# Kernel tuning notes

Measured on AMD Instinct MI355X. Metric: run time of the kernel, lower is better.

The kernel has to match this reference:

```python
import jax, jax.numpy as jnp
import numpy as np

NUM_HEADS = 16
LN_EPS = 1e-05


def setup_inputs() -> dict:
    key = jax.random.key(0)
    ks = jax.random.split(key, 10)
    B, S, H = 2, 2048, 1024
    s = 1.0 / np.sqrt(H)
    return {
        "hidden_states": jax.random.normal(ks[0], (B, S, H), dtype=jnp.float32),
        "Wq": jax.random.normal(ks[1], (H, H), dtype=jnp.float32) * s,
        "bq": jax.random.normal(ks[2], (H,), dtype=jnp.float32) * 0.02,
        "Wk": jax.random.normal(ks[3], (H, H), dtype=jnp.float32) * s,
        "bk": jax.random.normal(ks[4], (H,), dtype=jnp.float32) * 0.02,
        "Wv": jax.random.normal(ks[5], (H, H), dtype=jnp.float32) * s,
        "bv": jax.random.normal(ks[6], (H,), dtype=jnp.float32) * 0.02,
        "Wd": jax.random.normal(ks[7], (H, H), dtype=jnp.float32) * s,
        "bd": jax.random.normal(ks[8], (H,), dtype=jnp.float32) * 0.02,
        "ln_gamma": jnp.ones((H,), dtype=jnp.float32),
        "ln_beta": jnp.zeros((H,), dtype=jnp.float32),
    }


def reference(hidden_states, Wq, bq, Wk, bk, Wv, bv, Wd, bd, ln_gamma, ln_beta):
    B, S, H = hidden_states.shape
    nh = NUM_HEADS
    hd = H // nh

    # QKV projections (torch Linear: x @ W.T + b), split heads -> [B, nh, S, hd]
    def proj(W, b):
        y = jnp.einsum('bsh,oh->bso', hidden_states, W) + b
        return y.reshape(B, S, nh, hd).transpose(0, 2, 1, 3)

    q = proj(Wq, bq)
    k = proj(Wk, bk)
    v = proj(Wv, bv)

    # scaled dot-product attention: [B, nh, S, S]
    scores = jnp.einsum('bhqd,bhkd->bhqk', q, k) / jnp.sqrt(jnp.float32(hd))
    probs = jax.nn.softmax(scores, axis=-1)
    ctx = jnp.einsum('bhqk,bhkd->bhqd', probs, v)  # [B, nh, S, hd]
    ctx = ctx.transpose(0, 2, 1, 3).reshape(B, S, H)

    # output dense + residual + LayerNorm
    attn_out = jnp.einsum('bsh,oh->bso', ctx, Wd) + bd
    x = attn_out + hidden_states
    mu = jnp.mean(x, axis=-1, keepdims=True)
    var = jnp.mean(jnp.square(x - mu), axis=-1, keepdims=True)
    return (x - mu) * jax.lax.rsqrt(var + LN_EPS) * ln_gamma + ln_beta
```

## Files before the change

### kernel.cpp

```cpp
#include <hip/hip_runtime.h>

constexpr int kH    = 1024;
constexpr int kSEQ  = 2048;
constexpr int kBATCH= 2;
constexpr int kNH   = 16;
constexpr int kHD   = 64;
constexpr int kM    = 4096;

typedef _Float16 h8  __attribute__((ext_vector_type(8)));
typedef _Float16 h4  __attribute__((ext_vector_type(4)));
typedef float   f32x4 __attribute__((ext_vector_type(4)));

static __device__ __forceinline__ f32x4 mfma16(h8 a, h8 b, f32x4 c) {
  return __builtin_amdgcn_mfma_f32_16x16x32_f16(a, b, c, 0, 0, 0);
}

static __device__ __forceinline__ void gll16(const _Float16* g, _Float16* l) {
  __builtin_amdgcn_global_load_lds(
      (const __attribute__((address_space(1))) void*)g,
      (__attribute__((address_space(3))) void*)l, 16, 0, 0);
}

#define QSCALE 0.18033688011112042f
#define C0INIT (-5.770780163555854f)

__global__ __launch_bounds__(256) void cvt_all(
    const float* __restrict__ X,  const float* __restrict__ Wq,
    const float* __restrict__ Wk, const float* __restrict__ Wv,
    const float* __restrict__ Wd,
    _Float16* __restrict__ Xh,  _Float16* __restrict__ Wqh,
    _Float16* __restrict__ Wkh, _Float16* __restrict__ Wvh,
    _Float16* __restrict__ Wdh)
{
  int i = blockIdx.x * 256 + threadIdx.x;
  const float* src; _Float16* dst; int off;
  if (i < (kM * kH) / 4) {
    src = X; dst = Xh; off = i;
  } else {
    int j = i - (kM * kH) / 4;
    int w = j >> 18;
    off = j & 262143;
    src = (w == 0) ? Wq : (w == 1) ? Wk : (w == 2) ? Wv : Wd;
    dst = (w == 0) ? Wqh : (w == 1) ? Wkh : (w == 2) ? Wvh : Wdh;
  }
  float4 v = reinterpret_cast<const float4*>(src)[off];
  h4 o;
  o[0] = (_Float16)v.x; o[1] = (_Float16)v.y;
  o[2] = (_Float16)v.z; o[3] = (_Float16)v.w;
  reinterpret_cast<h4*>(dst)[off] = o;
}

__global__ __launch_bounds__(256, 3) void qkv_gemm(
    const _Float16* __restrict__ Xh,
    const _Float16* __restrict__ Wq, const _Float16* __restrict__ Wk,
    const _Float16* __restrict__ Wv,
    const float* __restrict__ bq, const float* __restrict__ bk,
    const float* __restrict__ bv,
    _Float16* __restrict__ Qo, _Float16* __restrict__ Ko, _Float16* __restrict__ Vo)
{
  const int bid = blockIdx.x;
  const int swz = (bid & 7) * 96 + (bid >> 3);
  const int bx  = swz & 7;
  const int rem = swz >> 3;
  const int by  = rem & 31;
  const int proj= rem >> 5;

  const _Float16* W   = (proj == 0) ? Wq : ((proj == 1) ? Wk : Wv);
  const float*    bias= (proj == 0) ? bq : ((proj == 1) ? bk : bv);
  _Float16*       Out = (proj == 0) ? Qo : ((proj == 1) ? Ko : Vo);

  const int m0 = by * 128, n0 = bx * 128;
  __shared__ __align__(16) char qsmem[32768];
  _Float16* const As = (_Float16*)qsmem;
  _Float16* const Bs = (_Float16*)(qsmem + 16384);
  _Float16* const Lt = (_Float16*)qsmem;

  const int tid  = threadIdx.x;
  const int wave = tid >> 6, lane = tid & 63, quad = lane >> 4, l16 = lane & 15;
  const int mw = (wave & 1) * 64, nw = (wave >> 1) * 64;

  f32x4 acc[4][4] = {};
  const int grow = wave * 32 + (lane >> 2);
  const int gcol = (lane & 3) * 8;
  const _Float16* Ag = Xh + (size_t)(m0 + grow) * kH + gcol;
  const _Float16* Bg = W  + (size_t)(n0 + grow) * kH + gcol;

  {
    gll16(Ag,            &As[wave * 1024]);
    gll16(Ag + 16 * kH,  &As[wave * 1024 + 512]);
    gll16(Bg,            &Bs[wave * 1024]);
    gll16(Bg + 16 * kH,  &Bs[wave * 1024 + 512]);
  }

  for (int k = 0; k < 32; ++k) {
    const int cur = k & 1;
    __syncthreads();
    if (k < 31) {
      const int k0 = (k + 1) * 32, nb = cur ^ 1;
      gll16(Ag + k0,           &As[nb * 4096 + wave * 1024]);
      gll16(Ag + 16 * kH + k0, &As[nb * 4096 + wave * 1024 + 512]);
      gll16(Bg + k0,           &Bs[nb * 4096 + wave * 1024]);
      gll16(Bg + 16 * kH + k0, &Bs[nb * 4096 + wave * 1024 + 512]);
    }
    h8 af[4], bf[4];
    #pragma unroll
    for (int mi = 0; mi < 4; ++mi)
      af[mi] = *reinterpret_cast<const h8*>(&As[cur * 4096 + (mw + mi * 16 + l16) * 32 + quad * 8]);
    #pragma unroll
    for (int ni = 0; ni < 4; ++ni)
      bf[ni] = *reinterpret_cast<const h8*>(&Bs[cur * 4096 + (nw + ni * 16 + l16) * 32 + quad * 8]);
    #pragma unroll
    for (int mi = 0; mi < 4; ++mi)
      #pragma unroll
      for (int ni = 0; ni < 4; ++ni)
        acc[mi][ni] = mfma16(af[mi], bf[ni], acc[mi][ni]);
  }

  if (proj != 2) {
    #pragma unroll
    for (int mi = 0; mi < 4; ++mi)
    #pragma unroll
    for (int ni = 0; ni < 4; ++ni) {
      const int ng = n0 + nw + ni * 16 + l16;
      const float bv_ = bias[ng];
      const int hh = ng >> 6, dd = ng & 63;
      #pragma unroll
      for (int r = 0; r < 4; ++r) {
        const int mg = m0 + mw + mi * 16 + quad * 4 + r;
        float val = acc[mi][ni][r] + bv_;
        if (proj == 0) val *= QSCALE;
        const int bb = mg >> 11, srow = mg & 2047;
        Out[(((size_t)(bb * kNH + hh) * kSEQ) + srow) * kHD + dd] = (_Float16)val;
      }
    }
  } else {
    __syncthreads();
    #pragma unroll
    for (int mi = 0; mi < 4; ++mi)
    #pragma unroll
    for (int ni = 0; ni < 4; ++ni) {
      const int ng = n0 + nw + ni * 16 + l16;
      const float bv_ = bias[ng];
      const int nl = nw + ni * 16 + l16;
      const int c16 = (mw >> 3) + mi * 2 + (quad >> 1);
      const int cs = c16 ^ (nl & 15);
      h4 pp;
      pp[0] = (_Float16)(acc[mi][ni][0] + bv_);
      pp[1] = (_Float16)(acc[mi][ni][1] + bv_);
      pp[2] = (_Float16)(acc[mi][ni][2] + bv_);
      pp[3] = (_Float16)(acc[mi][ni][3] + bv_);
      *reinterpret_cast<h4*>(&Lt[nl * 128 + cs * 8 + (quad & 1) * 4]) = pp;
    }
    __syncthreads();
    const int bb = m0 >> 11, srow0 = m0 & 2047;
    const int nl2 = tid >> 1, half = tid & 1;
    const int ng2 = n0 + nl2, hh2 = ng2 >> 6, dd2 = ng2 & 63;
    _Float16* dst = Out + ((size_t)(bb * kNH + hh2) * kHD + dd2) * kSEQ
                        + srow0 + half * 64;
    const int hperm = dd2 & 15;
    const int hx = hperm >> 1;
    const bool hswap = (hperm & 1);
    #pragma unroll
    for (int j = 0; j < 8; ++j) {
      const int c = half * 8 + j;
      const int cs = c ^ (nl2 & 15);
      h8 v = *reinterpret_cast<const h8*>(&Lt[nl2 * 128 + cs * 8]);
      if (hswap) {
        h8 vs;
        vs[0] = v[4]; vs[1] = v[5]; vs[2] = v[6]; vs[3] = v[7];
        vs[4] = v[0]; vs[5] = v[1]; vs[6] = v[2]; vs[7] = v[3];
        v = vs;
      }
      *reinterpret_cast<h8*>(dst + (j ^ hx) * 8) = v;
    }
  }
}

__global__ __launch_bounds__(512, 4) void attn_kernel(
    const _Float16* __restrict__ Q, const _Float16* __restrict__ K,
    const _Float16* __restrict__ Vt, _Float16* __restrict__ Ctx)
{
  const int bid = blockIdx.x;
  const int swzb = (bid & 7) * 64 + (bid >> 3);
  const int qt = swzb & 15, bh = swzb >> 4;
  const int tid = threadIdx.x;
  const int wave = tid >> 6, lane = tid & 63, quad = lane >> 4, l16 = lane & 15;
  const int sw = l16 & 7;
  const int qw = wave & 3;
  const int wg = wave >> 2;

  __shared__ __align__(16) char smem[49152];
  _Float16* const Kl = (_Float16*)smem;
  _Float16* const Vl = (_Float16*)(smem + 24576);
  float* const Ored = (float*)smem;
  float* const Lred = (float*)(smem + 34816);

  const _Float16* Qb = Q  + (size_t)bh * kSEQ * kHD;
  const _Float16* Kb = K  + (size_t)bh * kSEQ * kHD;
  const _Float16* Vb = Vt + (size_t)bh * kHD * kSEQ;

  const int qbase = qt * 128 + qw * 32;
  h8 qf[2][2];
  #pragma unroll
  for (int qh = 0; qh < 2; ++qh)
    #pragma unroll
    for (int dh = 0; dh < 2; ++dh)
      qf[qh][dh] = *reinterpret_cast<const h8*>(
          &Qb[(size_t)(qbase + qh * 16 + l16) * kHD + dh * 32 + quad * 8]);

  const int srow0  = lane >> 3;
  const int schunk = (lane & 7) ^ srow0;
  const int krow   = wave * 8 + srow0;
  const _Float16* Kg = Kb + (size_t)krow * kHD + schunk * 8;
  const _Float16* Vg = Vb + (size_t)krow * kSEQ + (lane & 7) * 8;

  const int slotA = 8 * wg + quad;
  const int offA = ((slotA    ) ^ l16) << 2;
  const int offB = ((slotA + 4) ^ l16) << 2;

  float l_acc[2] = {0.f, 0.f};
  f32x4 o[2][4] = {};

  auto STAGE = [&](int kt2, int buf) {
    const size_t ko = (size_t)kt2 * 64;
    gll16(Kg + ko * kHD, &Kl[buf * 4096 + (wave * 8) * 64]);
    gll16(Vg + ko,       &Vl[buf * 4096 + (wave * 8) * 64]);
  };

  auto COMPUTE = [&](const _Float16* Kc, const _Float16* Vc) {
    h8 ka[2][2];
    #pragma unroll
    for (int nt = 0; nt < 2; ++nt) {
      const int keyl = wg * 32 + nt * 16 + l16;
      ka[nt][0] = *reinterpret_cast<const h8*>(&Kc[keyl * 64 + ((quad    ) ^ sw) * 8]);
      ka[nt][1] = *reinterpret_cast<const h8*>(&Kc[keyl * 64 + ((quad ^ 4) ^ sw) * 8]);
    }
    f32x4 s[2][2];
    __builtin_amdgcn_s_setprio(1);
    #pragma unroll
    for (int nt = 0; nt < 2; ++nt)
      #pragma unroll
      for (int qh = 0; qh < 2; ++qh) {
        f32x4 a = {C0INIT, C0INIT, C0INIT, C0INIT};
        a = mfma16(ka[nt][0], qf[qh][0], a);
        a = mfma16(ka[nt][1], qf[qh][1], a);
        s[nt][qh] = a;
      }
    __builtin_amdgcn_s_setprio(0);

    h8 pa[2];
    #pragma unroll
    for (int qh = 0; qh < 2; ++qh) {
      float e00 = __builtin_amdgcn_exp2f(s[0][qh][0]);
      float e01 = __builtin_amdgcn_exp2f(s[0][qh][1]);
      float e02 = __builtin_amdgcn_exp2f(s[0][qh][2]);
      float e03 = __builtin_amdgcn_exp2f(s[0][qh][3]);
      float e10 = __builtin_amdgcn_exp2f(s[1][qh][0]);
      float e11 = __builtin_amdgcn_exp2f(s[1][qh][1]);
      float e12 = __builtin_amdgcn_exp2f(s[1][qh][2]);
      float e13 = __builtin_amdgcn_exp2f(s[1][qh][3]);
      l_acc[qh] += ((e00 + e01) + (e02 + e03)) + ((e10 + e11) + (e12 + e13));
      h8 p;
      p[0] = (_Float16)e00; p[1] = (_Float16)e01;
      p[2] = (_Float16)e02; p[3] = (_Float16)e03;
      p[4] = (_Float16)e10; p[5] = (_Float16)e11;
      p[6] = (_Float16)e12; p[7] = (_Float16)e13;
      pa[qh] = p;
    }

    __builtin_amdgcn_s_setprio(1);
    #pragma unroll
    for (int dt = 0; dt < 4; ++dt) {
      const _Float16* vr = &Vc[(dt * 16 + l16) * 64];
      h4 va  = *reinterpret_cast<const h4*>(vr + offA);
      h4 vbb = *reinterpret_cast<const h4*>(vr + offB);
      h8 v8 = __builtin_shufflevector(va, vbb, 0, 1, 2, 3, 4, 5, 6, 7);
      o[0][dt] = mfma16(pa[0], v8, o[0][dt]);
      o[1][dt] = mfma16(pa[1], v8, o[1][dt]);
    }
    __builtin_amdgcn_s_setprio(0);
  };

  STAGE(0, 0);
  STAGE(1, 1);

  int cur = 0;
  for (int kt = 0; kt < 30; ++kt) {
    asm volatile("s_waitcnt vmcnt(2)" ::: "memory");
    __builtin_amdgcn_sched_barrier(0);
    __builtin_amdgcn_s_barrier();
    __builtin_amdgcn_sched_barrier(0);
    int nb = cur + 2; if (nb >= 3) nb -= 3;
    STAGE(kt + 2, nb);
    COMPUTE(Kl + cur * 4096, Vl + cur * 4096);
    cur = (cur + 1 == 3) ? 0 : cur + 1;
  }
  asm volatile("s_waitcnt vmcnt(2)" ::: "memory");
  __builtin_amdgcn_sched_barrier(0);
  __builtin_amdgcn_s_barrier();
  __builtin_amdgcn_sched_barrier(0);
  COMPUTE(Kl + cur * 4096, Vl + cur * 4096);
  cur = (cur + 1 == 3) ? 0 : cur + 1;
  asm volatile("s_waitcnt vmcnt(0)" ::: "memory");
  __builtin_amdgcn_sched_barrier(0);
  __builtin_amdgcn_s_barrier();
  __builtin_amdgcn_sched_barrier(0);
  COMPUTE(Kl + cur * 4096, Vl + cur * 4096);

  float li[2] = {l_acc[0], l_acc[1]};
  #pragma unroll
  for (int qh = 0; qh < 2; ++qh) {
    li[qh] += __shfl_xor(li[qh], 16);
    li[qh] += __shfl_xor(li[qh], 32);
  }

  __syncthreads();
  if (wg == 1) {
    float* myO = Ored + (qw * 64 + lane) * 34;
    #pragma unroll
    for (int qh = 0; qh < 2; ++qh)
      #pragma unroll
      for (int dt = 0; dt < 4; ++dt) {
        reinterpret_cast<float2*>(&myO[qh * 16 + dt * 4])[0] =
            reinterpret_cast<const float2*>(&o[qh][dt])[0];
        reinterpret_cast<float2*>(&myO[qh * 16 + dt * 4 + 2])[0] =
            reinterpret_cast<const float2*>(&o[qh][dt])[1];
      }
    if (quad == 0) {
      Lred[(qw * 2 + 0) * 16 + l16] = li[0];
      Lred[(qw * 2 + 1) * 16 + l16] = li[1];
    }
  }
  __syncthreads();
  if (wg == 1) return;

  const float* pO = Ored + (qw * 64 + lane) * 34;
  #pragma unroll
  for (int qh = 0; qh < 2; ++qh) {
    #pragma unroll
    for (int dt = 0; dt < 4; ++dt) {
      float2 a = reinterpret_cast<const float2*>(&pO[qh * 16 + dt * 4])[0];
      float2 b2 = reinterpret_cast<const float2*>(&pO[qh * 16 + dt * 4 + 2])[0];
      o[qh][dt][0] += a.x;  o[qh][dt][1] += a.y;
      o[qh][dt][2] += b2.x; o[qh][dt][3] += b2.y;
    }
    li[qh] = 1.f / (li[qh] + Lred[(qw * 2 + qh) * 16 + l16]);
  }
  const int b = bh >> 4, hh = bh & 15;
  #pragma unroll
  for (int qh = 0; qh < 2; ++qh)
    #pragma unroll
    for (int r = 0; r < 4; ++r) {
      const float linv = __shfl(li[qh], quad * 4 + r);
      const int srow = qbase + qh * 16 + quad * 4 + r;
      #pragma unroll
      for (int dt = 0; dt < 4; ++dt) {
        const int col = hh * kHD + dt * 16 + l16;
        Ctx[((size_t)(b * kSEQ + srow)) * kH + col] = (_Float16)(o[qh][dt][r] * linv);
      }
    }
}

__global__ __launch_bounds__(256, 2) void dense_gemm(
    const _Float16* __restrict__ A, const _Float16* __restrict__ W,
    const float* __restrict__ bias, const _Float16* __restrict__ resid,
    _Float16* __restrict__ Out)
{
  const int bid = blockIdx.x;
  const int swz = (bid & 7) * 64 + (bid >> 3);
  const int bx  = swz & 15;
  const int by  = swz >> 4;
  const int m0 = by * 128, n0 = bx * 64;
  __shared__ __align__(16) _Float16 As[2][128 * 32];
  __shared__ __align__(16) _Float16 Bs[2][64 * 32];
  const int tid  = threadIdx.x;
  const int wave = tid >> 6, lane = tid & 63, quad = lane >> 4, l16 = lane & 15;
  const int mw = (wave & 1) * 64, nw = (wave >> 1) * 32;
  f32x4 acc[4][2] = {};
  const int growA = wave * 32 + (lane >> 2);
  const int growB = wave * 16 + (lane >> 2);
  const int gcol = (lane & 3) * 8;
  const _Float16* Ag = A + (size_t)(m0 + growA) * kH + gcol;
  const _Float16* Bg = W + (size_t)(n0 + growB) * kH + gcol;

  {
    gll16(Ag,           &As[0][wave * 1024]);
    gll16(Ag + 16 * kH, &As[0][wave * 1024 + 512]);
    gll16(Bg,           &Bs[0][wave * 512]);
  }

  for (int k = 0; k < 32; ++k) {
    const int cur = k & 1;
    __syncthreads();
    if (k < 31) {
      const int k0 = (k + 1) * 32, nb = cur ^ 1;
      gll16(Ag + k0,           &As[nb][wave * 1024]);
      gll16(Ag + 16 * kH + k0, &As[nb][wave * 1024 + 512]);
      gll16(Bg + k0,           &Bs[nb][wave * 512]);
    }
    h8 af[4], bf[2];
    #pragma unroll
    for (int mi = 0; mi < 4; ++mi)
      af[mi] = *reinterpret_cast<const h8*>(&As[cur][(mw + mi * 16 + l16) * 32 + quad * 8]);
    #pragma unroll
    for (int ni = 0; ni < 2; ++ni)
      bf[ni] = *reinterpret_cast<const h8*>(&Bs[cur][(nw + ni * 16 + l16) * 32 + quad * 8]);
    #pragma unroll
    for (int mi = 0; mi < 4; ++mi)
      #pragma unroll
      for (int ni = 0; ni < 2; ++ni)
        acc[mi][ni] = mfma16(af[mi], bf[ni], acc[mi][ni]);
  }
  #pragma unroll
  for (int mi = 0; mi < 4; ++mi)
  #pragma unroll
  for (int ni = 0; ni < 2; ++ni) {
    const int ng = n0 + nw + ni * 16 + l16;
    const float bv_ = bias[ng];
    #pragma unroll
    for (int r = 0; r < 4; ++r) {
      const int mg = m0 + mw + mi * 16 + quad * 4 + r;
      const float rs = (float)resid[(size_t)mg * kH + ng];
      Out[(size_t)mg * kH + ng] = (_Float16)(acc[mi][ni][r] + bv_ + rs);
    }
  }
}

__global__ __launch_bounds__(256) void ln_kernel(const _Float16* __restrict__ Tmp,
    const float* __restrict__ gamma, const float* __restrict__ beta,
    float* __restrict__ out)
{
  const int row = blockIdx.x;
  const h4 hv = reinterpret_cast<const h4*>(Tmp + (size_t)row * kH)[threadIdx.x];
  float vx = (float)hv[0], vy = (float)hv[1], vz = (float)hv[2], vw = (float)hv[3];
  float s  = vx + vy + vz + vw;
  float ss = vx * vx + vy * vy + vz * vz + vw * vw;
  #pragma unroll
  for (int off = 32; off > 0; off >>= 1) {
    s  += __shfl_down(s, off);
    ss += __shfl_down(ss, off);
  }
  __shared__ float red[8];
  const int wave = threadIdx.x >> 6, lane = threadIdx.x & 63;
  if (lane == 0) { red[wave] = s; red[4 + wave] = ss; }
  __syncthreads();
  s  = red[0] + red[1] + red[2] + red[3];
  ss = red[4] + red[5] + red[6] + red[7];
  const float mu   = s * (1.f / kH);
  const float var  = ss * (1.f / kH) - mu * mu;
  const float rstd = rsqrtf(var + 1e-5f);
  const float4 g  = reinterpret_cast<const float4*>(gamma)[threadIdx.x];
  const float4 bb = reinterpret_cast<const float4*>(beta)[threadIdx.x];
  float4 o;
  o.x = (vx - mu) * rstd * g.x + bb.x;
  o.y = (vy - mu) * rstd * g.y + bb.y;
  o.z = (vz - mu) * rstd * g.z + bb.z;
  o.w = (vw - mu) * rstd * g.w + bb.w;
  reinterpret_cast<float4*>(out + (size_t)row * kH)[threadIdx.x] = o;
}

extern "C" void kernel_launch(void* const* d_in, const int* in_sizes, int n_in,
                              void* d_out, int out_size, void* d_ws, size_t ws_size,
                              hipStream_t stream) {
  const float* hs    = (const float*)d_in[0];
  const float* Wq    = (const float*)d_in[1];
  const float* bq    = (const float*)d_in[2];
  const float* Wk    = (const float*)d_in[3];
  const float* bk    = (const float*)d_in[4];
  const float* Wv    = (const float*)d_in[5];
  const float* bv    = (const float*)d_in[6];
  const float* Wd    = (const float*)d_in[7];
  const float* bd    = (const float*)d_in[8];
  const float* gamma = (const float*)d_in[9];
  const float* beta  = (const float*)d_in[10];
  float* out = (float*)d_out;

  char* ws = (char*)d_ws;
  _Float16* Xh  = (_Float16*)(ws + 0);
  _Float16* Wqh = (_Float16*)(ws + 8388608);
  _Float16* Wkh = (_Float16*)(ws + 10485760);
  _Float16* Wvh = (_Float16*)(ws + 12582912);
  _Float16* Wdh = (_Float16*)(ws + 14680064);
  _Float16* Qh  = (_Float16*)(ws + 16777216);
  _Float16* Kh  = (_Float16*)(ws + 25165824);
  _Float16* Vth = (_Float16*)(ws + 33554432);
  _Float16* Ch  = (_Float16*)(ws + 41943040);
  _Float16* Tmp = Qh;

  cvt_all<<<8192, 256, 0, stream>>>(hs, Wq, Wk, Wv, Wd, Xh, Wqh, Wkh, Wvh, Wdh);
  qkv_gemm<<<768, 256, 0, stream>>>(
      Xh, Wqh, Wkh, Wvh, bq, bk, bv, Qh, Kh, Vth);
  attn_kernel<<<512, 512, 0, stream>>>(Qh, Kh, Vth, Ch);
  dense_gemm<<<512, 256, 0, stream>>>(Ch, Wdh, bd, Xh, Tmp);
  ln_kernel<<<kM, 256, 0, stream>>>(Tmp, gamma, beta, out);
}
```

Before: 198.6 us.

## Halve attention query tile to 64 rows and double-buffer K/V with syncthreads

Result: no change. 202.2 us (+1.8%).

```diff
diff --git a/kernel.cpp b/kernel.cpp
--- a/kernel.cpp
+++ b/kernel.cpp
@@ -176,37 +176,35 @@
   }
 }
 
-__global__ __launch_bounds__(512, 4) void attn_kernel(
+__global__ __launch_bounds__(512, 8) void attn_kernel(
     const _Float16* __restrict__ Q, const _Float16* __restrict__ K,
     const _Float16* __restrict__ Vt, _Float16* __restrict__ Ctx)
 {
   const int bid = blockIdx.x;
-  const int swzb = (bid & 7) * 64 + (bid >> 3);
-  const int qt = swzb & 15, bh = swzb >> 4;
+  const int swzb = (bid & 7) * 128 + (bid >> 3);
+  const int qt = swzb & 31, bh = swzb >> 5;
   const int tid = threadIdx.x;
   const int wave = tid >> 6, lane = tid & 63, quad = lane >> 4, l16 = lane & 15;
   const int sw = l16 & 7;
   const int qw = wave & 3;
   const int wg = wave >> 2;
 
-  __shared__ __align__(16) char smem[49152];
+  __shared__ __align__(16) char smem[32768];
   _Float16* const Kl = (_Float16*)smem;
-  _Float16* const Vl = (_Float16*)(smem + 24576);
+  _Float16* const Vl = (_Float16*)(smem + 16384);
   float* const Ored = (float*)smem;
-  float* const Lred = (float*)(smem + 34816);
+  float* const Lred = (float*)(smem + 18432);
 
   const _Float16* Qb = Q  + (size_t)bh * kSEQ * kHD;
   const _Float16* Kb = K  + (size_t)bh * kSEQ * kHD;
   const _Float16* Vb = Vt + (size_t)bh * kHD * kSEQ;
 
-  const int qbase = qt * 128 + qw * 32;
-  h8 qf[2][2];
-  #pragma unroll
-  for (int qh = 0; qh < 2; ++qh)
-    #pragma unroll
-    for (int dh = 0; dh < 2; ++dh)
-      qf[qh][dh] = *reinterpret_cast<const h8*>(
-          &Qb[(size_t)(qbase + qh * 16 + l16) * kHD + dh * 32 + quad * 8]);
+  const int qbase = qt * 64 + qw * 16;
+  h8 qf[2];
+  #pragma unroll
+  for (int dh = 0; dh < 2; ++dh)
+    qf[dh] = *reinterpret_cast<const h8*>(
+        &Qb[(size_t)(qbase + l16) * kHD + dh * 32 + quad * 8]);
 
   const int srow0  = lane >> 3;
   const int schunk = (lane & 7) ^ srow0;
@@ -218,16 +216,24 @@
   const int offA = ((slotA    ) ^ l16) << 2;
   const int offB = ((slotA + 4) ^ l16) << 2;
 
-  float l_acc[2] = {0.f, 0.f};
-  f32x4 o[2][4] = {};
-
-  auto STAGE = [&](int kt2, int buf) {
-    const size_t ko = (size_t)kt2 * 64;
-    gll16(Kg + ko * kHD, &Kl[buf * 4096 + (wave * 8) * 64]);
-    gll16(Vg + ko,       &Vl[buf * 4096 + (wave * 8) * 64]);
-  };
-
-  auto COMPUTE = [&](const _Float16* Kc, const _Float16* Vc) {
+  float l_acc = 0.f;
+  f32x4 o[4] = {};
+
+  gll16(Kg, &Kl[(wave * 8) * 64]);
+  gll16(Vg, &Vl[(wave * 8) * 64]);
+
+  for (int kt = 0; kt < kSEQ / 64; ++kt) {
+    const int cur = kt & 1;
+    __syncthreads();
+    if (kt + 1 < kSEQ / 64) {
+      const int nb = cur ^ 1;
+      const size_t ko = (size_t)(kt + 1) * 64;
+      gll16(Kg + ko * kHD, &Kl[nb * 4096 + (wave * 8) * 64]);
+      gll16(Vg + ko,       &Vl[nb * 4096 + (wave * 8) * 64]);
+    }
+    const _Float16* Kc = Kl + cur * 4096;
+    const _Float16* Vc = Vl + cur * 4096;
+
     h8 ka[2][2];
     #pragma unroll
     for (int nt = 0; nt < 2; ++nt) {
@@ -235,38 +241,31 @@
       ka[nt][0] = *reinterpret_cast<const h8*>(&Kc[keyl * 64 + ((quad    ) ^ sw) * 8]);
       ka[nt][1] = *reinterpret_cast<const h8*>(&Kc[keyl * 64 + ((quad ^ 4) ^ sw) * 8]);
     }
-    f32x4 s[2][2];
+    f32x4 s[2];
     __builtin_amdgcn_s_setprio(1);
     #pragma unroll
-    for (int nt = 0; nt < 2; ++nt)
-      #pragma unroll
-      for (int qh = 0; qh < 2; ++qh) {
-        f32x4 a = {C0INIT, C0INIT, C0INIT, C0INIT};
-        a = mfma16(ka[nt][0], qf[qh][0], a);
-        a = mfma16(ka[nt][1], qf[qh][1], a);
-        s[nt][qh] = a;
-      }
+    for (int nt = 0; nt < 2; ++nt) {
+      f32x4 a = {C0INIT, C0INIT, C0INIT, C0INIT};
+      a = mfma16(ka[nt][0], qf[0], a);
+      a = mfma16(ka[nt][1], qf[1], a);
+      s[nt] = a;
+    }
     __builtin_amdgcn_s_setprio(0);
 
-    h8 pa[2];
-    #pragma unroll
-    for (int qh = 0; qh < 2; ++qh) {
-      float e00 = __builtin_amdgcn_exp2f(s[0][qh][0]);
-      float e01 = __builtin_amdgcn_exp2f(s[0][qh][1]);
-      float e02 = __builtin_amdgcn_exp2f(s[0][qh][2]);
-      float e03 = __builtin_amdgcn_exp2f(s[0][qh][3]);
-      float e10 = __builtin_amdgcn_exp2f(s[1][qh][0]);
-      float e11 = __builtin_amdgcn_exp2f(s[1][qh][1]);
-      float e12 = __builtin_amdgcn_exp2f(s[1][qh][2]);
-      float e13 = __builtin_amdgcn_exp2f(s[1][qh][3]);
-      l_acc[qh] += ((e00 + e01) + (e02 + e03)) + ((e10 + e11) + (e12 + e13));
-      h8 p;
-      p[0] = (_Float16)e00; p[1] = (_Float16)e01;
-      p[2] = (_Float16)e02; p[3] = (_Float16)e03;
-      p[4] = (_Float16)e10; p[5] = (_Float16)e11;
-      p[6] = (_Float16)e12; p[7] = (_Float16)e13;
-      pa[qh] = p;
-    }
+    float e00 = __builtin_amdgcn_exp2f(s[0][0]);
+    float e01 = __builtin_amdgcn_exp2f(s[0][1]);
+    float e02 = __builtin_amdgcn_exp2f(s[0][2]);
+    float e03 = __builtin_amdgcn_exp2f(s[0][3]);
+    float e10 = __builtin_amdgcn_exp2f(s[1][0]);
+    float e11 = __builtin_amdgcn_exp2f(s[1][1]);
+    float e12 = __builtin_amdgcn_exp2f(s[1][2]);
+    float e13 = __builtin_amdgcn_exp2f(s[1][3]);
+    l_acc += ((e00 + e01) + (e02 + e03)) + ((e10 + e11) + (e12 + e13));
+    h8 pa;
+    pa[0] = (_Float16)e00; pa[1] = (_Float16)e01;
+    pa[2] = (_Float16)e02; pa[3] = (_Float16)e03;
+    pa[4] = (_Float16)e10; pa[5] = (_Float16)e11;
+    pa[6] = (_Float16)e12; pa[7] = (_Float16)e13;
 
     __builtin_amdgcn_s_setprio(1);
     #pragma unroll
@@ -275,90 +274,50 @@
       h4 va  = *reinterpret_cast<const h4*>(vr + offA);
       h4 vbb = *reinterpret_cast<const h4*>(vr + offB);
       h8 v8 = __builtin_shufflevector(va, vbb, 0, 1, 2, 3, 4, 5, 6, 7);
-      o[0][dt] = mfma16(pa[0], v8, o[0][dt]);
-      o[1][dt] = mfma16(pa[1], v8, o[1][dt]);
+      o[dt] = mfma16(pa, v8, o[dt]);
     }
     __builtin_amdgcn_s_setprio(0);
-  };
-
-  STAGE(0, 0);
-  STAGE(1, 1);
-
-  int cur = 0;
-  for (int kt = 0; kt < 30; ++kt) {
-    asm volatile("s_waitcnt vmcnt(2)" ::: "memory");
-    __builtin_amdgcn_sched_barrier(0);
-    __builtin_amdgcn_s_barrier();
-    __builtin_amdgcn_sched_barrier(0);
-    int nb = cur + 2; if (nb >= 3) nb -= 3;
-    STAGE(kt + 2, nb);
-    COMPUTE(Kl + cur * 4096, Vl + cur * 4096);
-    cur = (cur + 1 == 3) ? 0 : cur + 1;
-  }
-  asm volatile("s_waitcnt vmcnt(2)" ::: "memory");
-  __builtin_amdgcn_sched_barrier(0);
-  __builtin_amdgcn_s_barrier();
-  __builtin_amdgcn_sched_barrier(0);
-  COMPUTE(Kl + cur * 4096, Vl + cur * 4096);
-  cur = (cur + 1 == 3) ? 0 : cur + 1;
-  asm volatile("s_waitcnt vmcnt(0)" ::: "memory");
-  __builtin_amdgcn_sched_barrier(0);
-  __builtin_amdgcn_s_barrier();
-  __builtin_amdgcn_sched_barrier(0);
-  COMPUTE(Kl + cur * 4096, Vl + cur * 4096);
-
-  float li[2] = {l_acc[0], l_acc[1]};
-  #pragma unroll
-  for (int qh = 0; qh < 2; ++qh) {
-    li[qh] += __shfl_xor(li[qh], 16);
-    li[qh] += __shfl_xor(li[qh], 32);
-  }
+  }
+
+  float li = l_acc;
+  li += __shfl_xor(li, 16);
+  li += __shfl_xor(li, 32);
 
   __syncthreads();
   if (wg == 1) {
-    float* myO = Ored + (qw * 64 + lane) * 34;
-    #pragma unroll
-    for (int qh = 0; qh < 2; ++qh)
-      #pragma unroll
-      for (int dt = 0; dt < 4; ++dt) {
-        reinterpret_cast<float2*>(&myO[qh * 16 + dt * 4])[0] =
-            reinterpret_cast<const float2*>(&o[qh][dt])[0];
-        reinterpret_cast<float2*>(&myO[qh * 16 + dt * 4 + 2])[0] =
-            reinterpret_cast<const float2*>(&o[qh][dt])[1];
-      }
-    if (quad == 0) {
-      Lred[(qw * 2 + 0) * 16 + l16] = li[0];
-      Lred[(qw * 2 + 1) * 16 + l16] = li[1];
-    }
+    float* myO = Ored + (qw * 64 + lane) * 18;
+    #pragma unroll
+    for (int dt = 0; dt < 4; ++dt) {
+      reinterpret_cast<float2*>(&myO[dt * 4])[0] =
+          reinterpret_cast<const float2*>(&o[dt])[0];
+      reinterpret_cast<float2*>(&myO[dt * 4 + 2])[0] =
+          reinterpret_cast<const float2*>(&o[dt])[1];
+    }
+    if (quad == 0) Lred[qw * 16 + l16] = li;
   }
   __syncthreads();
   if (wg == 1) return;
 
-  const float* pO = Ored + (qw * 64 + lane) * 34;
-  #pragma unroll
-  for (int qh = 0; qh < 2; ++qh) {
+  const float* pO = Ored + (qw * 64 + lane) * 18;
+  #pragma unroll
+  for (int dt = 0; dt < 4; ++dt) {
+    float2 a  = reinterpret_cast<const float2*>(&pO[dt * 4])[0];
+    float2 b2 = reinterpret_cast<const float2*>(&pO[dt * 4 + 2])[0];
+    o[dt][0] += a.x;  o[dt][1] += a.y;
+    o[dt][2] += b2.x; o[dt][3] += b2.y;
+  }
+  li = 1.f / (li + Lred[qw * 16 + l16]);
+  const int b = bh >> 4, hh = bh & 15;
+  #pragma unroll
+  for (int r = 0; r < 4; ++r) {
+    const float linv = __shfl(li, quad * 4 + r);
+    const int srow = qbase + quad * 4 + r;
     #pragma unroll
     for (int dt = 0; dt < 4; ++dt) {
-      float2 a = reinterpret_cast<const float2*>(&pO[qh * 16 + dt * 4])[0];
-      float2 b2 = reinterpret_cast<const float2*>(&pO[qh * 16 + dt * 4 + 2])[0];
-      o[qh][dt][0] += a.x;  o[qh][dt][1] += a.y;
-      o[qh][dt][2] += b2.x; o[qh][dt][3] += b2.y;
-    }
-    li[qh] = 1.f / (li[qh] + Lred[(qw * 2 + qh) * 16 + l16]);
-  }
-  const int b = bh >> 4, hh = bh & 15;
-  #pragma unroll
-  for (int qh = 0; qh < 2; ++qh)
-    #pragma unroll
-    for (int r = 0; r < 4; ++r) {
-      const float linv = __shfl(li[qh], quad * 4 + r);
-      const int srow = qbase + qh * 16 + quad * 4 + r;
-      #pragma unroll
-      for (int dt = 0; dt < 4; ++dt) {
-        const int col = hh * kHD + dt * 16 + l16;
-        Ctx[((size_t)(b * kSEQ + srow)) * kH + col] = (_Float16)(o[qh][dt][r] * linv);
-      }
-    }
+      const int col = hh * kHD + dt * 16 + l16;
+      Ctx[((size_t)(b * kSEQ + srow)) * kH + col] = (_Float16)(o[dt][r] * linv);
+    }
+  }
 }
 
 __global__ __launch_bounds__(256, 2) void dense_gemm(
@@ -490,7 +449,7 @@
   cvt_all<<<8192, 256, 0, stream>>>(hs, Wq, Wk, Wv, Wd, Xh, Wqh, Wkh, Wvh, Wdh);
   qkv_gemm<<<768, 256, 0, stream>>>(
       Xh, Wqh, Wkh, Wvh, bq, bk, bv, Qh, Kh, Vth);
-  attn_kernel<<<512, 512, 0, stream>>>(Qh, Kh, Vth, Ch);
+  attn_kernel<<<1024, 512, 0, stream>>>(Qh, Kh, Vth, Ch);
   dense_gemm<<<512, 256, 0, stream>>>(Ch, Wdh, bd, Xh, Tmp);
   ln_kernel<<<kM, 256, 0, stream>>>(Tmp, gamma, beta, out);
 }
```
